# Performance work log

Hardware: AMD Instinct MI355X
Metric: run time of the kernel (lower is better)

Reference implementation:

```python
import jax, jax.numpy as jnp
import numpy as np
from jax import lax

B, NMEAS, M, LAYER_NUM = 2048, 128, 256, 10
CLAMP_MIN, CLAMP_MAX = 1e-6, 100.0
EPS_S = 1e-6


def _conv2d(x, w, b):
    y = lax.conv_general_dilated(x, w, (1, 1), 'SAME', dimension_numbers=('NCHW', 'OIHW', 'NCHW'))
    return y + b[None, :, None, None]


def _conv1d(x, w, b):
    y = lax.conv_general_dilated(x, w, (1,), 'SAME', dimension_numbers=('NCH', 'OIH', 'NCH'))
    return y + b[None, :, None]


def setup_inputs():
    key = jax.random.key(0)
    ks = jax.random.split(key, 12)
    s = 1.0 / np.sqrt(2.0 * NMEAS)  # ~unit-norm dictionary columns
    return {
        'Yr': jax.random.normal(ks[0], (B, 1, NMEAS, 1), jnp.float32),
        'Yi': jax.random.normal(ks[1], (B, 1, NMEAS, 1), jnp.float32),
        'Ar': s * jax.random.normal(ks[2], (NMEAS, M), jnp.float32),
        'Ai': s * jax.random.normal(ks[3], (NMEAS, M), jnp.float32),
        'conv1_w': 0.1 * jax.random.normal(ks[4], (32, 2, 3, 3), jnp.float32),
        'conv1_b': jnp.zeros((32,), jnp.float32),
        'conv2_w': 0.1 * jax.random.normal(ks[5], (64, 32, 3, 3), jnp.float32),
        'conv2_b': jnp.zeros((64,), jnp.float32),
        'hc_w': 0.1 * jax.random.normal(ks[6], (LAYER_NUM - 1, 64, 3), jnp.float32),
        'hc_b': jnp.zeros((LAYER_NUM - 1,), jnp.float32),
        'hd_w': 0.1 * jax.random.normal(ks[7], (LAYER_NUM - 1, 64, 3), jnp.float32),
        'hd_b': jnp.zeros((LAYER_NUM - 1,), jnp.float32),
        'hT_w': 0.1 * jax.random.normal(ks[8], (LAYER_NUM, 64, 3), jnp.float32),
        'hT_b': jnp.zeros((LAYER_NUM,), jnp.float32),
        'a0': jnp.asarray(1.0, jnp.float32),
        'b0': jnp.asarray(1.0, jnp.float32),
    }


def _hypernet(ay, c1w, c1b, c2w, c2b, hcw, hcb, hdw, hdb, hTw, hTb):
    # ay: [B, 2, M]; batch acts as image width (context)
    x_img = jnp.transpose(ay, (1, 2, 0))[None]              # [1, 2, M, B]
    f = jax.nn.relu(_conv2d(x_img, c1w, c1b))               # [1, 32, M, B]
    f = jax.nn.relu(_conv2d(f, c2w, c2b))                   # [1, 64, M, B]
    f = jnp.mean(f, axis=2)                                 # AdaptiveAvgPool2d((1,None)) -> [1, 64, B]
    c = jnp.abs(_conv1d(f, hcw, hcb))[0].T                  # [B, L-1]
    d = jnp.abs(_conv1d(f, hdw, hdb))[0].T                  # [B, L-1]
    T = jnp.abs(_conv1d(f, hTw, hTb))[0].T                  # [B, L]
    c = jnp.clip(c, CLAMP_MIN, CLAMP_MAX)
    d = jnp.maximum(d, CLAMP_MIN)
    T = jnp.clip(T, CLAMP_MIN, CLAMP_MAX)
    return c, d, T


def _forward(Yr, Yi, Ar, Ai, conv1_w, conv1_b, conv2_w, conv2_b,
             hc_w, hc_b, hd_w, hd_b, hT_w, hT_b, a0, b0):
    Y = (Yr + 1j * Yi).astype(jnp.complex64)                # [B,1,Nmeas,1]
    A = (Ar + 1j * Ai).astype(jnp.complex64)                # [Nmeas,M]
    AT = A.conj().T                                         # [M,Nmeas]
    AA = AT @ A                                             # [M,M] Hermitian
    AY = jnp.matmul(AT, Y)                                  # [B,1,M,1]
    b = Y.shape[0]
    n = Y.shape[2]
    ay = jnp.concatenate([AY.real.reshape(b, 1, -1), AY.imag.reshape(b, 1, -1)], axis=1)  # [B,2,M]
    c, d, T = _hypernet(ay, conv1_w, conv1_b, conv2_w, conv2_b,
                        hc_w, hc_b, hd_w, hd_b, hT_w, hT_b)
    D = jnp.real(jnp.diagonal(AA))[None, None, :, None]     # diag of Hermitian AA is real; [1,1,M,1]
    eps = (a0 / b0).astype(jnp.complex64) * jnp.ones((b, 1, 1, 1), jnp.complex64)
    Lam = ((c[:, 0] / d[:, 0])[:, None, None, None] * jnp.ones((1, 1, M, 1), jnp.float32)).astype(jnp.complex64)
    U = jnp.zeros((b, 1, M, 1), jnp.complex64)
    a = a0 + n
    for k in range(LAYER_NUM - 1):
        Tk = T[:, k][:, None, None, None]
        # fused SBL/VAMP mean update
        U = eps * (Tk * U - jnp.matmul(AA, U) + AY) / (eps * Tk + Lam + EPS_S)
        Sigma = 1.0 / (eps * D + Lam + EPS_S)
        r = Y - jnp.matmul(A, U)
        eps1 = jnp.sum(r.real ** 2 + r.imag ** 2, axis=(2, 3), keepdims=True)  # ||.||_F^2
        eps2 = jnp.sum(D * Sigma, axis=(2, 3), keepdims=True)
        eps = a / (b0 + eps1 + eps2 + EPS_S)
        Lam = (c[:, k][:, None, None, None] + 1.0) / (
            d[:, k][:, None, None, None] + jnp.abs(U) ** 2 + Sigma + EPS_S)
    Tk = T[:, LAYER_NUM - 1][:, None, None, None]
    U = eps * (Tk * U - jnp.matmul(AA, U) + AY) / (eps * Tk + Lam + EPS_S)
    Ua = jnp.abs(U)
    Ua = Ua / (jnp.max(Ua) + 1e-8)
    return Ua, c, d, T


def reference(Yr, Yi, Ar, Ai, conv1_w, conv1_b, conv2_w, conv2_b,
              hc_w, hc_b, hd_w, hd_b, hT_w, hT_b, a0, b0):
    Ua, c, d, T = _forward(Yr, Yi, Ar, Ai, conv1_w, conv1_b, conv2_w, conv2_b,
                           hc_w, hc_b, hd_w, hd_b, hT_w, hT_b, a0, b0)
    # original returns the last batch row of c/d/T (detached diagnostics)
    return Ua, c[-1:, :], d[-1:, :], T[-1:, :]
```

## Files before the change

kernel.cpp:

```cpp
#include <hip/hip_runtime.h>
#include <math.h>

#define B_N   2048
#define NM    128
#define M_N   256
#define LNUM  10
#define EPS_Sf 1e-6f

typedef _Float16 half8 __attribute__((ext_vector_type(8)));
typedef float floatx4 __attribute__((ext_vector_type(4)));

__device__ __forceinline__ float frcp(float x) { return __builtin_amdgcn_rcpf(x); }

static constexpr size_t o_AA  = 0;
static constexpr size_t o_D   = o_AA  + 131072;
static constexpr size_t o_yn  = o_D   + 256;
static constexpr size_t o_AY  = o_yn  + 2048;
static constexpr size_t o_AYt = o_AY  + 1048576;
static constexpr size_t o_w2t = o_AYt + 1048576;
static constexpr size_t o_z1  = o_w2t + 18432;
static constexpr size_t o_fp  = o_z1  + 16777216;
static constexpr size_t o_f   = o_fp  + 2097152;
static constexpr size_t o_c   = o_f   + 131072;
static constexpr size_t o_dd  = o_c   + 18432;
static constexpr size_t o_T   = o_dd  + 18432;
static constexpr size_t o_Ua  = o_T   + 20480;
static constexpr size_t o_gm  = o_Ua  + 524288;

#define Z1T_RS (2050 * 32)

__global__ void k_pre(const float* __restrict__ Ar, const float* __restrict__ Ai,
                      const float* __restrict__ Yr, const float* __restrict__ Yi,
                      const float* __restrict__ w2, float* __restrict__ ws) {
    __shared__ float sb[2048];
    int blk = blockIdx.x;
    int tid = threadIdx.x;
    if (blk < 256) {
        float* cr = sb; float* ci = sb + NM;
        int i = blk, j = tid;
        if (j < NM) { cr[j] = Ar[j * M_N + i]; ci[j] = Ai[j * M_N + i]; }
        __syncthreads();
        float sr = 0.f, si = 0.f;
        for (int n = 0; n < NM; ++n) {
            float ar = Ar[n * M_N + j], ai = Ai[n * M_N + j];
            sr += cr[n] * ar + ci[n] * ai;
            si += cr[n] * ai - ci[n] * ar;
        }
        _Float16* A16 = (_Float16*)(ws + o_AA);
        size_t off = ((size_t)((i >> 4) * 8 + (j >> 5)) * 64
                      + (size_t)(((j >> 3) & 3) * 16 + (i & 15))) * 8 + (j & 7);
        A16[off]         = (_Float16)sr;
        A16[65536 + off] = (_Float16)si;
        if (j == i) ws[o_D + i] = sr;
        if (i == 0 && j == 0) *(unsigned int*)(ws + o_gm) = 0u;
    } else if (blk < 328) {
        int i = (blk - 256) * 256 + tid;
        if (i < 64 * 32 * 9) {
            int oc = i / 288, r = i % 288;
            int ic = r / 9, kk = r % 9;
            _Float16* Wa = (_Float16*)(ws + o_w2t);
            Wa[((size_t)oc * 9 + kk) * 32 + ic] = (_Float16)w2[i];
        }
    } else {
        float2* Ys = (float2*)sb;
        int bb0 = (blk - 328) * 8;
        for (int i = tid; i < 8 * NM; i += 256) {
            int g = i >> 7, n = i & 127;
            Ys[g * NM + n] = make_float2(Yr[(size_t)(bb0 + g) * NM + n],
                                         Yi[(size_t)(bb0 + g) * NM + n]);
        }
        __syncthreads();
        if (tid < 8) {
            float s = 0.f;
            for (int n = 0; n < NM; ++n) { float2 y = Ys[tid * NM + n]; s += y.x * y.x + y.y * y.y; }
            ws[o_yn + bb0 + tid] = s;
        }
        int m = tid;
        float accr[8], acci[8];
#pragma unroll
        for (int g = 0; g < 8; ++g) { accr[g] = 0.f; acci[g] = 0.f; }
        for (int n = 0; n < NM; ++n) {
            float ar = Ar[n * M_N + m], ai = Ai[n * M_N + m];
#pragma unroll
            for (int g = 0; g < 8; ++g) {
                float2 y = Ys[g * NM + n];
                accr[g] += ar * y.x + ai * y.y;
                acci[g] += ar * y.y - ai * y.x;
            }
        }
        float2* AY = (float2*)(ws + o_AY);
#pragma unroll
        for (int g = 0; g < 8; ++g) {
            AY[(size_t)(bb0 + g) * M_N + m] = make_float2(accr[g], acci[g]);
            ws[o_AYt + (size_t)m * B_N + (bb0 + g)] = accr[g];
            ws[o_AYt + 524288 + (size_t)m * B_N + (bb0 + g)] = acci[g];
        }
    }
}

__global__ void k_conv1(const float* __restrict__ w1, const float* __restrict__ b1,
                        float* __restrict__ ws) {
    __shared__ float w1s[576], b1s[32];
    int tid = threadIdx.x;
    for (int i = tid; i < 576; i += 256) w1s[i] = w1[i];
    if (tid < 32) b1s[tid] = b1[tid];
    __syncthreads();
    int gidx = blockIdx.x * 256 + tid;
    int b = gidx & (B_N - 1), m = gidx >> 11;
    const float* xr = ws + o_AYt;
    float x[2][3][3];
#pragma unroll
    for (int c = 0; c < 2; ++c)
#pragma unroll
        for (int dm = 0; dm < 3; ++dm) {
            int mm = m + dm - 1;
#pragma unroll
            for (int db = 0; db < 3; ++db) {
                int bb = b + db - 1;
                x[c][dm][db] = (mm >= 0 && mm < M_N && bb >= 0 && bb < B_N)
                                 ? xr[(size_t)c * 524288 + (size_t)mm * B_N + bb] : 0.f;
            }
        }
    _Float16* z1t = (_Float16*)(ws + o_z1);
    _Float16 zv[32];
    for (int oc = 0; oc < 32; ++oc) {
        float acc = b1s[oc];
#pragma unroll
        for (int c = 0; c < 2; ++c)
#pragma unroll
            for (int dm = 0; dm < 3; ++dm)
#pragma unroll
                for (int db = 0; db < 3; ++db)
                    acc += x[c][dm][db] * w1s[oc * 18 + c * 9 + dm * 3 + db];
        zv[oc] = (_Float16)fmaxf(acc, 0.f);
    }
    _Float16* dst = z1t + (size_t)(m + 1) * Z1T_RS + (size_t)(b + 1) * 32;
#pragma unroll
    for (int v = 0; v < 4; ++v) *(half8*)(dst + v * 8) = *(half8*)(zv + v * 8);
    half8 z8 = (half8)((_Float16)0.f);
    if (m == 0) {
        _Float16* d2 = z1t + (size_t)(b + 1) * 32;
#pragma unroll
        for (int v = 0; v < 4; ++v) *(half8*)(d2 + v * 8) = z8;
        if (b == 0) { _Float16* d3 = z1t;
#pragma unroll
            for (int v = 0; v < 4; ++v) *(half8*)(d3 + v * 8) = z8; }
        if (b == B_N - 1) { _Float16* d3 = z1t + (size_t)2049 * 32;
#pragma unroll
            for (int v = 0; v < 4; ++v) *(half8*)(d3 + v * 8) = z8; }
    }
    if (m == M_N - 1) {
        _Float16* d2 = z1t + (size_t)257 * Z1T_RS + (size_t)(b + 1) * 32;
#pragma unroll
        for (int v = 0; v < 4; ++v) *(half8*)(d2 + v * 8) = z8;
        if (b == 0) { _Float16* d3 = z1t + (size_t)257 * Z1T_RS;
#pragma unroll
            for (int v = 0; v < 4; ++v) *(half8*)(d3 + v * 8) = z8; }
        if (b == B_N - 1) { _Float16* d3 = z1t + (size_t)257 * Z1T_RS + (size_t)2049 * 32;
#pragma unroll
            for (int v = 0; v < 4; ++v) *(half8*)(d3 + v * 8) = z8; }
    }
    if (b == 0) {
        _Float16* d2 = z1t + (size_t)(m + 1) * Z1T_RS;
#pragma unroll
        for (int v = 0; v < 4; ++v) *(half8*)(d2 + v * 8) = z8;
    }
    if (b == B_N - 1) {
        _Float16* d2 = z1t + (size_t)(m + 1) * Z1T_RS + (size_t)2049 * 32;
#pragma unroll
        for (int v = 0; v < 4; ++v) *(half8*)(d2 + v * 8) = z8;
    }
}

#define MFMA16(A,Bv,C) C = __builtin_amdgcn_mfma_f32_16x16x32_f16(A, Bv, C, 0, 0, 0)
__global__ void __launch_bounds__(128)
k_conv2m(const float* __restrict__ b2, float* __restrict__ ws) {
    int tid = threadIdx.x;
    int lane = tid & 63, wv = tid >> 6;
    int col = lane & 15, quad = lane >> 4;
    int bt = blockIdx.x & 127, g = blockIdx.x >> 7;
    int b0 = bt * 16, m0 = g * 16;
    int oc0w = wv * 32;
    const _Float16* z1t = (const _Float16*)(ws + o_z1);
    const _Float16* Wa  = (const _Float16*)(ws + o_w2t);

    half8 Af[2][9];
#pragma unroll
    for (int t = 0; t < 2; ++t)
#pragma unroll
        for (int kk = 0; kk < 9; ++kk)
            Af[t][kk] = *(const half8*)(Wa + ((size_t)(oc0w + t * 16 + col) * 9 + kk) * 32 + quad * 8);
    float bias[2][4];
#pragma unroll
    for (int t = 0; t < 2; ++t)
#pragma unroll
        for (int r = 0; r < 4; ++r)
            bias[t][r] = b2[oc0w + t * 16 + quad * 4 + r];

    const _Float16* zb = z1t + (size_t)(b0 + col) * 32 + quad * 8;
    half8 Bf[3][3];
#pragma unroll
    for (int ph = 0; ph < 3; ++ph)
#pragma unroll
        for (int db = 0; db < 3; ++db)
            Bf[ph][db] = *(const half8*)(zb + (size_t)(m0 + ph) * Z1T_RS + (size_t)db * 32);

    floatx4 facc[2];
    facc[0] = (floatx4){0.f, 0.f, 0.f, 0.f};
    facc[1] = (floatx4){0.f, 0.f, 0.f, 0.f};

#pragma unroll
    for (int mm = 0; mm < 16; ++mm) {
        floatx4 a0 = (floatx4){0.f, 0.f, 0.f, 0.f};
        floatx4 a1 = (floatx4){0.f, 0.f, 0.f, 0.f};
#pragma unroll
        for (int dm = 0; dm < 3; ++dm) {
            int ph = (mm + dm) % 3;
#pragma unroll
            for (int db = 0; db < 3; ++db) {
                MFMA16(Af[0][dm * 3 + db], Bf[ph][db], a0);
                MFMA16(Af[1][dm * 3 + db], Bf[ph][db], a1);
            }
        }
#pragma unroll
        for (int r = 0; r < 4; ++r) {
            facc[0][r] += fmaxf(a0[r] + bias[0][r], 0.f);
            facc[1][r] += fmaxf(a1[r] + bias[1][r], 0.f);
        }
        if (mm < 15) {
            int ph = mm % 3;
#pragma unroll
            for (int db = 0; db < 3; ++db)
                Bf[ph][db] = *(const half8*)(zb + (size_t)(m0 + mm + 3) * Z1T_RS + (size_t)db * 32);
        }
    }
    float* fp = ws + o_fp + (size_t)g * 131072;
#pragma unroll
    for (int t = 0; t < 2; ++t)
#pragma unroll
        for (int r = 0; r < 4; ++r)
            fp[(size_t)(oc0w + t * 16 + quad * 4 + r) * B_N + b0 + col] = facc[t][r];
}

__global__ void k_fred(float* __restrict__ ws) {
    size_t i = (size_t)blockIdx.x * 256 + threadIdx.x;
    float s = 0.f;
    for (int p = 0; p < 16; ++p) s += ws[o_fp + (size_t)p * 131072 + i];
    ws[o_f + i] = s * (1.f / 256.f);
}

__global__ void k_cdt(const float* __restrict__ hcw, const float* __restrict__ hcb,
                      const float* __restrict__ hdw, const float* __restrict__ hdb,
                      const float* __restrict__ hTw, const float* __restrict__ hTb,
                      float* __restrict__ ws, float* __restrict__ out) {
    int l = blockIdx.x >> 3;
    int b = (blockIdx.x & 7) * 256 + threadIdx.x;
    const float* f = ws + o_f;
    const float* w; float bi; int li, kind;
    if (l < 9)       { kind = 0; li = l;      w = hcw + (size_t)li * 192; bi = hcb[li]; }
    else if (l < 18) { kind = 1; li = l - 9;  w = hdw + (size_t)li * 192; bi = hdb[li]; }
    else             { kind = 2; li = l - 18; w = hTw + (size_t)li * 192; bi = hTb[li]; }
    __shared__ float wsm[192];
    for (int i = threadIdx.x; i < 192; i += 256) wsm[i] = w[i];
    __syncthreads();
    float acc = bi;
    bool okL = (b > 0), okR = (b < B_N - 1);
    for (int ic = 0; ic < 64; ++ic) {
        const float* fr = f + (size_t)ic * B_N + b;
        float fm1 = okL ? fr[-1] : 0.f;
        float f0  = fr[0];
        float fp1 = okR ? fr[1] : 0.f;
        acc += fm1 * wsm[ic * 3] + f0 * wsm[ic * 3 + 1] + fp1 * wsm[ic * 3 + 2];
    }
    float v = fmaxf(fabsf(acc), 1e-6f);
    if (kind != 1) v = fminf(v, 100.f);
    if (kind == 0)      { ws[o_c  + (size_t)b * 9  + li] = v; if (b == B_N - 1) out[524288 + li] = v; }
    else if (kind == 1) { ws[o_dd + (size_t)b * 9  + li] = v; if (b == B_N - 1) out[524297 + li] = v; }
    else                { ws[o_T  + (size_t)b * 10 + li] = v; if (b == B_N - 1) out[524306 + li] = v; }
}

__global__ void __launch_bounds__(512, 2)
k_iter(const float* __restrict__ a0p, const float* __restrict__ b0p, float* __restrict__ ws) {
    __shared__ __align__(16) _Float16 Ubf[2][8][64][8];
    __shared__ __align__(16) float redv[16][28];
    __shared__ float redm[8];
    int tid = threadIdx.x;
    int lane = tid & 63, w = tid >> 6;
    int col = lane & 15, quad = lane >> 4;
    int b = blockIdx.x * 16 + col;

    for (int i = tid; i < 16 * 28; i += 512) ((float*)redv)[i] = 0.f;

    const float2* AY = (const float2*)(ws + o_AY);
    const _Float16* Af = (const _Float16*)(ws + o_AA);
    float a0 = a0p[0], b0v = b0p[0];
    float atot = a0 + (float)NM;
    float yn = ws[o_yn + b];
    float eps = a0 / b0v;

    half8 Ar8[2][8], Ai8[2][8];
#pragma unroll
    for (int t = 0; t < 2; ++t)
#pragma unroll
        for (int ks = 0; ks < 8; ++ks) {
            const _Float16* ab = Af + (((size_t)(w * 2 + t) * 8 + ks) * 64 + lane) * 8;
            Ar8[t][ks] = *(const half8*)(ab);
            Ai8[t][ks] = *(const half8*)(ab + 65536);
        }

    float Dv[8], ayr[8], ayi[8], lam[8], Ur[8], Ui[8];
    float c0h = ws[o_c + (size_t)b * 9];
    float d0h = ws[o_dd + (size_t)b * 9];
    float T0 = ws[o_T + (size_t)b * 10];
    float lam0 = c0h * frcp(d0h);
#pragma unroll
    for (int ri = 0; ri < 8; ++ri) {
        int m = w * 32 + (ri >> 2) * 16 + quad * 4 + (ri & 3);
        Dv[ri] = ws[o_D + m];
        float2 a = AY[(size_t)b * M_N + m];
        ayr[ri] = a.x; ayi[ri] = a.y;
        lam[ri] = lam0;
    }
    {
        float iv = eps * frcp(fmaf(eps, T0, lam0 + EPS_Sf));
#pragma unroll
        for (int ri = 0; ri < 8; ++ri) { Ur[ri] = iv * ayr[ri]; Ui[ri] = iv * ayi[ri]; }
    }

    int laneD0 = ((quad >> 1)) * 16 + col;
    int laneD1 = (2 + (quad >> 1)) * 16 + col;
    int eb = (quad & 1) * 4;

    for (int k = 0; k < LNUM - 1; ++k) {
        float ck = ws[o_c + (size_t)b * 9 + k];
        float dk = ws[o_dd + (size_t)b * 9 + k];
        float Tn = ws[o_T + (size_t)b * 10 + k + 1];
        {
            union { _Float16 h[4]; unsigned long long u; } pk;
#pragma unroll
            for (int t = 0; t < 2; ++t) {
                int ld = t ? laneD1 : laneD0;
#pragma unroll
                for (int r = 0; r < 4; ++r) pk.h[r] = (_Float16)Ur[t * 4 + r];
                *(unsigned long long*)&Ubf[0][w][ld][eb] = pk.u;
#pragma unroll
                for (int r = 0; r < 4; ++r) pk.h[r] = (_Float16)Ui[t * 4 + r];
                *(unsigned long long*)&Ubf[1][w][ld][eb] = pk.u;
            }
        }
        __syncthreads();
        floatx4 ac[8];
#pragma unroll
        for (int i = 0; i < 8; ++i) ac[i] = (floatx4){0.f, 0.f, 0.f, 0.f};
#pragma unroll
        for (int ks = 0; ks < 8; ++ks) {
            half8 urh = *(const half8*)&Ubf[0][ks][lane][0];
            half8 uih = *(const half8*)&Ubf[1][ks][lane][0];
            MFMA16(Ar8[0][ks], urh, ac[0]);
            MFMA16(Ai8[0][ks], uih, ac[1]);
            MFMA16(Ar8[0][ks], uih, ac[2]);
            MFMA16(Ai8[0][ks], urh, ac[3]);
            MFMA16(Ar8[1][ks], urh, ac[4]);
            MFMA16(Ai8[1][ks], uih, ac[5]);
            MFMA16(Ar8[1][ks], uih, ac[6]);
            MFMA16(Ai8[1][ks], urh, ac[7]);
        }
        float wr[8], wi[8], sg[8];
        float p1 = 0.f, p2 = 0.f, p3 = 0.f;
#pragma unroll
        for (int t = 0; t < 2; ++t)
#pragma unroll
            for (int r = 0; r < 4; ++r) {
                int ri = t * 4 + r;
                wr[ri] = ac[t * 4 + 0][r] - ac[t * 4 + 1][r];
                wi[ri] = ac[t * 4 + 2][r] + ac[t * 4 + 3][r];
                sg[ri] = frcp(fmaf(eps, Dv[ri], lam[ri] + EPS_Sf));
                p1 += ayr[ri] * Ur[ri] + ayi[ri] * Ui[ri];
                p2 += Ur[ri] * wr[ri] + Ui[ri] * wi[ri];
                p3 += Dv[ri] * sg[ri];
            }
        p1 += __shfl_xor(p1, 16); p1 += __shfl_xor(p1, 32);
        p2 += __shfl_xor(p2, 16); p2 += __shfl_xor(p2, 32);
        p3 += __shfl_xor(p3, 16); p3 += __shfl_xor(p3, 32);
        if (lane < 16) {
            redv[col][w * 3]     = p1;
            redv[col][w * 3 + 1] = p2;
            redv[col][w * 3 + 2] = p3;
        }
        __syncthreads();
        float s[3] = {0.f, 0.f, 0.f};
#pragma unroll
        for (int j = 0; j < 7; ++j) {
            floatx4 v4 = *(const floatx4*)&redv[col][j * 4];
#pragma unroll
            for (int e = 0; e < 4; ++e) s[(j * 4 + e) % 3] += v4[e];
        }
        float eps1 = fmaxf(yn - 2.f * s[0] + s[1], 0.f);
        eps = atot * frcp(b0v + eps1 + s[2] + EPS_Sf);
        float ck1 = ck + 1.f;
#pragma unroll
        for (int ri = 0; ri < 8; ++ri) {
            lam[ri] = ck1 * frcp(dk + Ur[ri] * Ur[ri] + Ui[ri] * Ui[ri] + sg[ri] + EPS_Sf);
            float iv = eps * frcp(fmaf(eps, Tn, lam[ri] + EPS_Sf));
            Ur[ri] = iv * (Tn * Ur[ri] - wr[ri] + ayr[ri]);
            Ui[ri] = iv * (Tn * Ui[ri] - wi[ri] + ayi[ri]);
        }
    }
    float lm = 0.f;
#pragma unroll
    for (int t = 0; t < 2; ++t) {
        float4 v;
        v.x = sqrtf(Ur[t * 4 + 0] * Ur[t * 4 + 0] + Ui[t * 4 + 0] * Ui[t * 4 + 0]);
        v.y = sqrtf(Ur[t * 4 + 1] * Ur[t * 4 + 1] + Ui[t * 4 + 1] * Ui[t * 4 + 1]);
        v.z = sqrtf(Ur[t * 4 + 2] * Ur[t * 4 + 2] + Ui[t * 4 + 2] * Ui[t * 4 + 2]);
        v.w = sqrtf(Ur[t * 4 + 3] * Ur[t * 4 + 3] + Ui[t * 4 + 3] * Ui[t * 4 + 3]);
        *(float4*)&ws[o_Ua + (size_t)b * M_N + w * 32 + t * 16 + quad * 4] = v;
        lm = fmaxf(lm, fmaxf(fmaxf(v.x, v.y), fmaxf(v.z, v.w)));
    }
#pragma unroll
    for (int off = 32; off >= 1; off >>= 1) lm = fmaxf(lm, __shfl_xor(lm, off));
    if (lane == 0) redm[w] = lm;
    __syncthreads();
    if (tid == 0) {
        float mx = redm[0];
#pragma unroll
        for (int i = 1; i < 8; ++i) mx = fmaxf(mx, redm[i]);
        atomicMax((unsigned int*)(ws + o_gm), __float_as_uint(mx));
    }
}

__global__ void k_norm(const float* __restrict__ ws, float* __restrict__ out) {
    size_t i = (size_t)blockIdx.x * 256 + threadIdx.x;
    float gm = __uint_as_float(*(const unsigned int*)(ws + o_gm));
    out[i] = ws[o_Ua + i] / (gm + 1e-8f);
}

extern "C" void kernel_launch(void* const* d_in, const int* in_sizes, int n_in,
                              void* d_out, int out_size, void* d_ws, size_t ws_size,
                              hipStream_t stream) {
    (void)in_sizes; (void)n_in; (void)out_size; (void)ws_size;
    const float* Yr  = (const float*)d_in[0];
    const float* Yi  = (const float*)d_in[1];
    const float* Ar  = (const float*)d_in[2];
    const float* Ai  = (const float*)d_in[3];
    const float* w1  = (const float*)d_in[4];
    const float* b1  = (const float*)d_in[5];
    const float* w2  = (const float*)d_in[6];
    const float* b2  = (const float*)d_in[7];
    const float* hcw = (const float*)d_in[8];
    const float* hcb = (const float*)d_in[9];
    const float* hdw = (const float*)d_in[10];
    const float* hdb = (const float*)d_in[11];
    const float* hTw = (const float*)d_in[12];
    const float* hTb = (const float*)d_in[13];
    const float* a0  = (const float*)d_in[14];
    const float* b0  = (const float*)d_in[15];
    float* ws = (float*)d_ws;
    float* out = (float*)d_out;

    k_pre   <<<584, 256, 0, stream>>>(Ar, Ai, Yr, Yi, w2, ws);
    k_conv1 <<<2048, 256, 0, stream>>>(w1, b1, ws);
    k_conv2m<<<2048, 128, 0, stream>>>(b2, ws);
    k_fred  <<<512, 256, 0, stream>>>(ws);
    k_cdt   <<<224, 256, 0, stream>>>(hcw, hcb, hdw, hdb, hTw, hTb, ws, out);
    k_iter  <<<128, 512, 0, stream>>>(a0, b0, ws);
    k_norm  <<<2048, 256, 0, stream>>>(ws, out);
}
```

Measured before the change: 229.4 us.

## Fuse conv1 into conv2 tile kernel via LDS halo and MFMA conv1

```diff
diff --git a/kernel.cpp b/kernel.cpp
--- a/kernel.cpp
+++ b/kernel.cpp
@@ -26,8 +26,6 @@
 static constexpr size_t o_T   = o_dd  + 18432;
 static constexpr size_t o_Ua  = o_T   + 20480;
 static constexpr size_t o_gm  = o_Ua  + 524288;
-
-#define Z1T_RS (2050 * 32)
 
 __global__ void k_pre(const float* __restrict__ Ar, const float* __restrict__ Ai,
                       const float* __restrict__ Yr, const float* __restrict__ Yi,
@@ -98,148 +96,125 @@
     }
 }
 
-__global__ void k_conv1(const float* __restrict__ w1, const float* __restrict__ b1,
-                        float* __restrict__ ws) {
-    __shared__ float w1s[576], b1s[32];
+#define MFMA16(A,Bv,C) C = __builtin_amdgcn_mfma_f32_16x16x32_f16(A, Bv, C, 0, 0, 0)
+__global__ void __launch_bounds__(256)
+k_conv12(const float* __restrict__ w1, const float* __restrict__ b1,
+         const float* __restrict__ b2, float* __restrict__ ws) {
+    __shared__ __align__(16) _Float16 zt[18 * 18 * 40];
     int tid = threadIdx.x;
-    for (int i = tid; i < 576; i += 256) w1s[i] = w1[i];
-    if (tid < 32) b1s[tid] = b1[tid];
-    __syncthreads();
-    int gidx = blockIdx.x * 256 + tid;
-    int b = gidx & (B_N - 1), m = gidx >> 11;
-    const float* xr = ws + o_AYt;
-    float x[2][3][3];
-#pragma unroll
-    for (int c = 0; c < 2; ++c)
-#pragma unroll
-        for (int dm = 0; dm < 3; ++dm) {
-            int mm = m + dm - 1;
-#pragma unroll
-            for (int db = 0; db < 3; ++db) {
-                int bb = b + db - 1;
-                x[c][dm][db] = (mm >= 0 && mm < M_N && bb >= 0 && bb < B_N)
-                                 ? xr[(size_t)c * 524288 + (size_t)mm * B_N + bb] : 0.f;
-            }
-        }
-    _Float16* z1t = (_Float16*)(ws + o_z1);
-    _Float16 zv[32];
-    for (int oc = 0; oc < 32; ++oc) {
-        float acc = b1s[oc];
-#pragma unroll
-        for (int c = 0; c < 2; ++c)
-#pragma unroll
-            for (int dm = 0; dm < 3; ++dm)
-#pragma unroll
-                for (int db = 0; db < 3; ++db)
-                    acc += x[c][dm][db] * w1s[oc * 18 + c * 9 + dm * 3 + db];
-        zv[oc] = (_Float16)fmaxf(acc, 0.f);
-    }
-    _Float16* dst = z1t + (size_t)(m + 1) * Z1T_RS + (size_t)(b + 1) * 32;
-#pragma unroll
-    for (int v = 0; v < 4; ++v) *(half8*)(dst + v * 8) = *(half8*)(zv + v * 8);
-    half8 z8 = (half8)((_Float16)0.f);
-    if (m == 0) {
-        _Float16* d2 = z1t + (size_t)(b + 1) * 32;
-#pragma unroll
-        for (int v = 0; v < 4; ++v) *(half8*)(d2 + v * 8) = z8;
-        if (b == 0) { _Float16* d3 = z1t;
-#pragma unroll
-            for (int v = 0; v < 4; ++v) *(half8*)(d3 + v * 8) = z8; }
-        if (b == B_N - 1) { _Float16* d3 = z1t + (size_t)2049 * 32;
-#pragma unroll
-            for (int v = 0; v < 4; ++v) *(half8*)(d3 + v * 8) = z8; }
-    }
-    if (m == M_N - 1) {
-        _Float16* d2 = z1t + (size_t)257 * Z1T_RS + (size_t)(b + 1) * 32;
-#pragma unroll
-        for (int v = 0; v < 4; ++v) *(half8*)(d2 + v * 8) = z8;
-        if (b == 0) { _Float16* d3 = z1t + (size_t)257 * Z1T_RS;
-#pragma unroll
-            for (int v = 0; v < 4; ++v) *(half8*)(d3 + v * 8) = z8; }
-        if (b == B_N - 1) { _Float16* d3 = z1t + (size_t)257 * Z1T_RS + (size_t)2049 * 32;
-#pragma unroll
-            for (int v = 0; v < 4; ++v) *(half8*)(d3 + v * 8) = z8; }
-    }
-    if (b == 0) {
-        _Float16* d2 = z1t + (size_t)(m + 1) * Z1T_RS;
-#pragma unroll
-        for (int v = 0; v < 4; ++v) *(half8*)(d2 + v * 8) = z8;
-    }
-    if (b == B_N - 1) {
-        _Float16* d2 = z1t + (size_t)(m + 1) * Z1T_RS + (size_t)2049 * 32;
-#pragma unroll
-        for (int v = 0; v < 4; ++v) *(half8*)(d2 + v * 8) = z8;
-    }
-}
-
-#define MFMA16(A,Bv,C) C = __builtin_amdgcn_mfma_f32_16x16x32_f16(A, Bv, C, 0, 0, 0)
-__global__ void __launch_bounds__(128)
-k_conv2m(const float* __restrict__ b2, float* __restrict__ ws) {
-    int tid = threadIdx.x;
-    int lane = tid & 63, wv = tid >> 6;
+    int lane = tid & 63, w = tid >> 6;
     int col = lane & 15, quad = lane >> 4;
     int bt = blockIdx.x & 127, g = blockIdx.x >> 7;
     int b0 = bt * 16, m0 = g * 16;
-    int oc0w = wv * 32;
-    const _Float16* z1t = (const _Float16*)(ws + o_z1);
-    const _Float16* Wa  = (const _Float16*)(ws + o_w2t);
-
-    half8 Af[2][9];
+
+    half8 Aw[2];
 #pragma unroll
     for (int t = 0; t < 2; ++t)
 #pragma unroll
-        for (int kk = 0; kk < 9; ++kk)
-            Af[t][kk] = *(const half8*)(Wa + ((size_t)(oc0w + t * 16 + col) * 9 + kk) * 32 + quad * 8);
-    float bias[2][4];
-#pragma unroll
-    for (int t = 0; t < 2; ++t)
-#pragma unroll
-        for (int r = 0; r < 4; ++r)
-            bias[t][r] = b2[oc0w + t * 16 + quad * 4 + r];
-
-    const _Float16* zb = z1t + (size_t)(b0 + col) * 32 + quad * 8;
+        for (int j = 0; j < 8; ++j) {
+            int k = quad * 8 + j;
+            int oc = t * 16 + col;
+            Aw[t][j] = (k < 18) ? (_Float16)w1[oc * 18 + (k & 1) * 9 + (k >> 1)]
+                                : (_Float16)0.f;
+        }
+    float b1a[4], b1b[4];
+#pragma unroll
+    for (int r = 0; r < 4; ++r) { b1a[r] = b1[quad * 4 + r]; b1b[r] = b1[16 + quad * 4 + r]; }
+
+    int dmj[8], dbj[8], offc[8];
+#pragma unroll
+    for (int j = 0; j < 8; ++j) {
+        int k = quad * 8 + j;
+        int e = k >> 1;
+        int dm = (e * 11) >> 5;
+        int db = e - dm * 3;
+        if (k >= 18) dm = 1 << 20;
+        dmj[j] = dm; dbj[j] = db;
+        offc[j] = (k & 1) * 524288;
+    }
+
+    const float* xr = ws + o_AYt;
+    for (int grp = w; grp < 21; grp += 4) {
+        int p = grp * 16 + col;
+        int mz = (p * 57) >> 10;
+        int bz = p - mz * 18;
+        int m_pt = m0 - 2 + mz, b_pt = b0 - 2 + bz;
+        bool pok = (p < 324);
+        half8 xb;
+#pragma unroll
+        for (int j = 0; j < 8; ++j) {
+            int row = m_pt + dmj[j], bc = b_pt + dbj[j];
+            bool ok = pok && ((unsigned)row < (unsigned)M_N) && ((unsigned)bc < (unsigned)B_N);
+            float v = ok ? xr[(size_t)offc[j] + (size_t)row * B_N + bc] : 0.f;
+            xb[j] = (_Float16)v;
+        }
+        floatx4 z0 = (floatx4){0.f, 0.f, 0.f, 0.f};
+        floatx4 z1v = (floatx4){0.f, 0.f, 0.f, 0.f};
+        MFMA16(Aw[0], xb, z0);
+        MFMA16(Aw[1], xb, z1v);
+        bool zok = ((unsigned)(m0 - 1 + mz) < (unsigned)M_N) &&
+                   ((unsigned)(b0 - 1 + bz) < (unsigned)B_N);
+        unsigned long long u0 = 0ull, u1 = 0ull;
+        if (zok) {
+            union { _Float16 h[4]; unsigned long long u; } a;
+#pragma unroll
+            for (int r = 0; r < 4; ++r) a.h[r] = (_Float16)fmaxf(z0[r] + b1a[r], 0.f);
+            u0 = a.u;
+#pragma unroll
+            for (int r = 0; r < 4; ++r) a.h[r] = (_Float16)fmaxf(z1v[r] + b1b[r], 0.f);
+            u1 = a.u;
+        }
+        if (pok) {
+            _Float16* d = zt + (size_t)(mz * 18 + bz) * 40 + quad * 4;
+            *(unsigned long long*)(d)      = u0;
+            *(unsigned long long*)(d + 16) = u1;
+        }
+    }
+
+    const _Float16* Wa = (const _Float16*)(ws + o_w2t);
+    int oc0w = w * 16;
+    half8 Af[9];
+#pragma unroll
+    for (int kk = 0; kk < 9; ++kk)
+        Af[kk] = *(const half8*)(Wa + ((size_t)(oc0w + col) * 9 + kk) * 32 + quad * 8);
+    float bias2[4];
+#pragma unroll
+    for (int r = 0; r < 4; ++r) bias2[r] = b2[oc0w + quad * 4 + r];
+
+    __syncthreads();
+
+    const _Float16* zb = zt + (size_t)col * 40 + (size_t)quad * 8;
     half8 Bf[3][3];
 #pragma unroll
     for (int ph = 0; ph < 3; ++ph)
 #pragma unroll
         for (int db = 0; db < 3; ++db)
-            Bf[ph][db] = *(const half8*)(zb + (size_t)(m0 + ph) * Z1T_RS + (size_t)db * 32);
-
-    floatx4 facc[2];
-    facc[0] = (floatx4){0.f, 0.f, 0.f, 0.f};
-    facc[1] = (floatx4){0.f, 0.f, 0.f, 0.f};
-
+            Bf[ph][db] = *(const half8*)(zb + (size_t)ph * 720 + (size_t)db * 40);
+
+    floatx4 facc = (floatx4){0.f, 0.f, 0.f, 0.f};
 #pragma unroll
     for (int mm = 0; mm < 16; ++mm) {
         floatx4 a0 = (floatx4){0.f, 0.f, 0.f, 0.f};
-        floatx4 a1 = (floatx4){0.f, 0.f, 0.f, 0.f};
 #pragma unroll
         for (int dm = 0; dm < 3; ++dm) {
             int ph = (mm + dm) % 3;
 #pragma unroll
-            for (int db = 0; db < 3; ++db) {
-                MFMA16(Af[0][dm * 3 + db], Bf[ph][db], a0);
-                MFMA16(Af[1][dm * 3 + db], Bf[ph][db], a1);
-            }
-        }
-#pragma unroll
-        for (int r = 0; r < 4; ++r) {
-            facc[0][r] += fmaxf(a0[r] + bias[0][r], 0.f);
-            facc[1][r] += fmaxf(a1[r] + bias[1][r], 0.f);
-        }
+            for (int db = 0; db < 3; ++db)
+                MFMA16(Af[dm * 3 + db], Bf[ph][db], a0);
+        }
+#pragma unroll
+        for (int r = 0; r < 4; ++r) facc[r] += fmaxf(a0[r] + bias2[r], 0.f);
         if (mm < 15) {
             int ph = mm % 3;
 #pragma unroll
             for (int db = 0; db < 3; ++db)
-                Bf[ph][db] = *(const half8*)(zb + (size_t)(m0 + mm + 3) * Z1T_RS + (size_t)db * 32);
+                Bf[ph][db] = *(const half8*)(zb + (size_t)(mm + 3) * 720 + (size_t)db * 40);
         }
     }
     float* fp = ws + o_fp + (size_t)g * 131072;
 #pragma unroll
-    for (int t = 0; t < 2; ++t)
-#pragma unroll
-        for (int r = 0; r < 4; ++r)
-            fp[(size_t)(oc0w + t * 16 + quad * 4 + r) * B_N + b0 + col] = facc[t][r];
+    for (int r = 0; r < 4; ++r)
+        fp[(size_t)(oc0w + quad * 4 + r) * B_N + b0 + col] = facc[r];
 }
 
 __global__ void k_fred(float* __restrict__ ws) {
@@ -459,8 +434,7 @@
     float* out = (float*)d_out;
 
     k_pre   <<<584, 256, 0, stream>>>(Ar, Ai, Yr, Yi, w2, ws);
-    k_conv1 <<<2048, 256, 0, stream>>>(w1, b1, ws);
-    k_conv2m<<<2048, 128, 0, stream>>>(b2, ws);
+    k_conv12<<<2048, 256, 0, stream>>>(w1, b1, b2, ws);
     k_fred  <<<512, 256, 0, stream>>>(ws);
     k_cdt   <<<224, 256, 0, stream>>>(hcw, hcb, hdw, hdb, hTw, hTb, ws, out);
     k_iter  <<<128, 512, 0, stream>>>(a0, b0, ws);
```

New measurement: 231.3 us. Within noise of the previous version (+0.8%).
